# Performance work log

Hardware: AMD Instinct MI355X
Metric: run time of the kernel (lower is better)

Reference implementation:

```python
import jax, jax.numpy as jnp
import numpy as np

B, S, E, H, F = 8, 1024, 1024, 16, 4096
D = E // H  # head_dim = 64
EPS = 1e-5


def setup_inputs() -> dict:
    key = jax.random.key(0)
    ks = jax.random.split(key, 12)
    s = 0.02
    return {
        "x": jax.random.normal(ks[0], (B, S, E), dtype=jnp.float32),
        # per-head projections (shared across heads), torch stores [out,in]; we use [in,out]
        "Wq": jax.random.normal(ks[1], (D, D), dtype=jnp.float32) * s,
        "Wk": jax.random.normal(ks[2], (D, D), dtype=jnp.float32) * s,
        "Wv": jax.random.normal(ks[3], (D, D), dtype=jnp.float32) * s,
        "Wo": jax.random.normal(ks[4], (E, E), dtype=jnp.float32) * s,
        "bo": jnp.zeros((E,), dtype=jnp.float32),
        "W1": jax.random.normal(ks[5], (E, F), dtype=jnp.float32) * s,
        "b1": jnp.zeros((F,), dtype=jnp.float32),
        "W2": jax.random.normal(ks[6], (F, E), dtype=jnp.float32) * s,
        "b2": jnp.zeros((E,), dtype=jnp.float32),
        "g1": jnp.ones((E,), dtype=jnp.float32),
        "beta1": jnp.zeros((E,), dtype=jnp.float32),
        "g2": jnp.ones((E,), dtype=jnp.float32),
        "beta2": jnp.zeros((E,), dtype=jnp.float32),
    }


def _layer_norm(x, g, b):
    m = jnp.mean(x, axis=-1, keepdims=True)
    v = jnp.mean(jnp.square(x - m), axis=-1, keepdims=True)
    return (x - m) * jax.lax.rsqrt(v + EPS) * g + b


def reference(x, Wq, Wk, Wv, Wo, bo, W1, b1, W2, b2, g1, beta1, g2, beta2):
    b, s, e = x.shape
    # --- attention sublayer (pre-norm) ---
    nx = _layer_norm(x, g1, beta1)
    h = nx.reshape(b, s, H, D)              # [B,S,H,D]
    q = h @ Wq                               # per-head linear, weight shared over heads
    k = h @ Wk
    v = h @ Wv
    energy = jnp.einsum('bqhd,bkhd->bhqk', q, k)  # full [B,H,S,S] scores
    mask = jnp.tril(jnp.ones((s, s), dtype=bool))
    energy = jnp.where(mask, energy, -jnp.inf)
    att = jax.nn.softmax(energy / jnp.sqrt(jnp.float32(e)), axis=-1)  # NOTE: scale by sqrt(embed_dim)
    o = jnp.einsum('bhqk,bkhd->bqhd', att, v).reshape(b, s, e)
    x = x + (o @ Wo + bo)
    # --- MLP sublayer (pre-norm); dropout is identity in eval ---
    nx = _layer_norm(x, g2, beta2)
    x = x + (jax.nn.relu(nx @ W1 + b1) @ W2 + b2)
    return x
```

## Files before the change

### kernel.cpp

```cpp
#include <hip/hip_runtime.h>

typedef unsigned short u16;
typedef __attribute__((ext_vector_type(4))) float f4;
typedef __attribute__((ext_vector_type(8))) short s8v;
typedef __attribute__((ext_vector_type(4))) unsigned short u16x4;

#define DEVINL __device__ __forceinline__

DEVINL float b2f(u16 u) { union { unsigned i; float f; } x; x.i = ((unsigned)u) << 16; return x.f; }
DEVINL u16 f2b(float f) {
  union { float f; unsigned i; } x; x.f = f;
  unsigned r = 0x7FFFu + ((x.i >> 16) & 1u);
  return (u16)((x.i + r) >> 16);
}

#define GLD_LDS16(g, l)                                                        \
  __builtin_amdgcn_global_load_lds((__attribute__((address_space(1))) void*)(g), \
                                   (__attribute__((address_space(3))) void*)(l), 16, 0, 0)

__global__ __launch_bounds__(256) void k_transpose(const float* __restrict__ in,
                                                   u16* __restrict__ out, int R, int C) {
  __shared__ float t[32][33];
  int tx = threadIdx.x & 31, ty = threadIdx.x >> 5;
  int c0 = blockIdx.x * 32, r0 = blockIdx.y * 32;
#pragma unroll
  for (int i = 0; i < 32; i += 8)
    t[ty + i][tx] = in[(long)(r0 + ty + i) * C + (c0 + tx)];
  __syncthreads();
#pragma unroll
  for (int i = 0; i < 32; i += 8)
    out[(long)(c0 + ty + i) * R + (r0 + tx)] = f2b(t[tx][ty + i]);
}

__global__ __launch_bounds__(256) void k_vtrans(const u16* __restrict__ v, u16* __restrict__ vt) {
  __shared__ u16 t[64][72];
  int bh = blockIdx.x, b = bh >> 4, h = bh & 15;
  int s0 = blockIdx.y * 64;
  int tid = threadIdx.x;
#pragma unroll
  for (int p = 0; p < 2; ++p) {
    int idx = p * 256 + tid;
    int sl = idx >> 3, c8 = (idx & 7) * 8;
    *(s8v*)(&t[sl][c8]) = *(const s8v*)(v + (((long)(b * 1024 + s0 + sl) * 16 + h) * 64) + c8);
  }
  __syncthreads();
#pragma unroll
  for (int p = 0; p < 2; ++p) {
    int idx = p * 256 + tid;
    int d = idx >> 3, c8 = (idx & 7) * 8;
    s8v o;
#pragma unroll
    for (int e = 0; e < 8; ++e) o[e] = (short)t[c8 + e][d];
    *(s8v*)(vt + ((long)bh * 64 + d) * 1024 + s0 + c8) = o;
  }
}

__global__ __launch_bounds__(256) void k_layernorm(const float* __restrict__ x,
                                                   const float* __restrict__ g,
                                                   const float* __restrict__ be,
                                                   u16* __restrict__ out) {
  long row = blockIdx.x;
  int tid = threadIdx.x;
  f4 v = ((const f4*)(x + row * 1024))[tid];
  float s = v[0] + v[1] + v[2] + v[3];
  float s2 = v[0] * v[0] + v[1] * v[1] + v[2] * v[2] + v[3] * v[3];
#pragma unroll
  for (int off = 32; off > 0; off >>= 1) {
    s += __shfl_down(s, off, 64);
    s2 += __shfl_down(s2, off, 64);
  }
  __shared__ float red[8];
  int wv = tid >> 6, ln = tid & 63;
  if (ln == 0) { red[wv] = s; red[4 + wv] = s2; }
  __syncthreads();
  s = red[0] + red[1] + red[2] + red[3];
  s2 = red[4] + red[5] + red[6] + red[7];
  float mean = s * (1.0f / 1024.0f);
  float var = s2 * (1.0f / 1024.0f) - mean * mean;
  float rs = rsqrtf(var + 1e-5f);
  f4 gg = ((const f4*)g)[tid];
  f4 bb = ((const f4*)be)[tid];
  u16x4 o;
#pragma unroll
  for (int i = 0; i < 4; ++i) o[i] = f2b((v[i] - mean) * rs * gg[i] + bb[i]);
  ((u16x4*)(out + row * 1024))[tid] = o;
}

__global__ __launch_bounds__(256) void k_qkv(const u16* __restrict__ nx, const u16* __restrict__ WqT,
                                             const u16* __restrict__ WkT, const u16* __restrict__ WvT,
                                             u16* __restrict__ q, u16* __restrict__ k,
                                             u16* __restrict__ v) {
  int tid = threadIdx.x, lane = tid & 63, wave = tid >> 6;
  int quad = lane >> 4, l16 = lane & 15;
  long rbase = (long)blockIdx.x * 64 + wave * 16;
  s8v a0 = *(const s8v*)(nx + (rbase + l16) * 64 + quad * 8);
  s8v a1 = *(const s8v*)(nx + (rbase + l16) * 64 + 32 + quad * 8);
  const u16* Ws[3] = {WqT, WkT, WvT};
  u16* Os[3] = {q, k, v};
#pragma unroll
  for (int t = 0; t < 3; ++t) {
#pragma unroll
    for (int j = 0; j < 4; ++j) {
      s8v b0 = *(const s8v*)(Ws[t] + (j * 16 + l16) * 64 + quad * 8);
      s8v b1 = *(const s8v*)(Ws[t] + (j * 16 + l16) * 64 + 32 + quad * 8);
      f4 acc = {0.f, 0.f, 0.f, 0.f};
      acc = __builtin_amdgcn_mfma_f32_16x16x32_bf16(a0, b0, acc, 0, 0, 0);
      acc = __builtin_amdgcn_mfma_f32_16x16x32_bf16(a1, b1, acc, 0, 0, 0);
#pragma unroll
      for (int r = 0; r < 4; ++r)
        Os[t][(rbase + quad * 4 + r) * 64 + j * 16 + l16] = f2b(acc[r]);
    }
  }
}

__global__ __launch_bounds__(256) void k_attn_mfma(const u16* __restrict__ q,
                                                   const u16* __restrict__ kk,
                                                   const u16* __restrict__ vt,
                                                   u16* __restrict__ o) {
  constexpr int LDK = 72;
  __shared__ u16 Ks[64 * LDK];
  __shared__ u16 Vt[64 * LDK];
  __shared__ u16 Ps[4][16 * LDK];
  int tid = threadIdx.x, lane = tid & 63, wave = tid >> 6;
  int quad = lane >> 4, l16 = lane & 15;
  int b = blockIdx.x >> 4, h = blockIdx.x & 15;
  int qi = (int)gridDim.y - 1 - (int)blockIdx.y;
  int q0 = qi * 64 + wave * 16;

  const u16* qp = q + (((long)(b * 1024 + q0 + l16)) * 16 + h) * 64;
  s8v aq0 = *(const s8v*)(qp + quad * 8);
  s8v aq1 = *(const s8v*)(qp + 32 + quad * 8);

  f4 O[4];
  float m_[4], l_[4];
#pragma unroll
  for (int jd = 0; jd < 4; ++jd) O[jd] = f4{0.f, 0.f, 0.f, 0.f};
#pragma unroll
  for (int r = 0; r < 4; ++r) { m_[r] = -__builtin_inff(); l_[r] = 0.f; }

  for (int kt = 0; kt <= qi; ++kt) {
    __syncthreads();
#pragma unroll
    for (int p = 0; p < 2; ++p) {
      int idx = p * 256 + tid;
      int row = idx >> 3, c8 = (idx & 7) * 8;
      *(s8v*)(Ks + row * LDK + c8) =
          *(const s8v*)(kk + (((long)(b * 1024 + kt * 64 + row)) * 16 + h) * 64 + c8);
      *(s8v*)(Vt + row * LDK + c8) =
          *(const s8v*)(vt + ((long)blockIdx.x * 64 + row) * 1024 + kt * 64 + c8);
    }
    __syncthreads();

    f4 sf[4];
#pragma unroll
    for (int jn = 0; jn < 4; ++jn) {
      s8v b0 = *(const s8v*)(Ks + (jn * 16 + l16) * LDK + quad * 8);
      s8v b1 = *(const s8v*)(Ks + (jn * 16 + l16) * LDK + 32 + quad * 8);
      f4 acc = f4{0.f, 0.f, 0.f, 0.f};
      acc = __builtin_amdgcn_mfma_f32_16x16x32_bf16(aq0, b0, acc, 0, 0, 0);
      acc = __builtin_amdgcn_mfma_f32_16x16x32_bf16(aq1, b1, acc, 0, 0, 0);
      sf[jn] = acc;
    }
    bool diag = (kt == qi);
    float rm[4];
#pragma unroll
    for (int r = 0; r < 4; ++r) rm[r] = -__builtin_inff();
#pragma unroll
    for (int jn = 0; jn < 4; ++jn)
#pragma unroll
      for (int r = 0; r < 4; ++r) {
        float v = sf[jn][r] * 0.03125f;
        if (diag && (jn * 16 + l16 > wave * 16 + quad * 4 + r)) v = -__builtin_inff();
        sf[jn][r] = v;
        rm[r] = fmaxf(rm[r], v);
      }
#pragma unroll
    for (int off = 1; off < 16; off <<= 1)
#pragma unroll
      for (int r = 0; r < 4; ++r) rm[r] = fmaxf(rm[r], __shfl_xor(rm[r], off, 64));
    float alpha[4], rs[4];
#pragma unroll
    for (int r = 0; r < 4; ++r) {
      float mn = fmaxf(m_[r], rm[r]);
      alpha[r] = __expf(m_[r] - mn);
      m_[r] = mn;
      rs[r] = 0.f;
    }
#pragma unroll
    for (int jn = 0; jn < 4; ++jn)
#pragma unroll
      for (int r = 0; r < 4; ++r) {
        float p = __expf(sf[jn][r] - m_[r]);
        rs[r] += p;
        Ps[wave][(quad * 4 + r) * LDK + jn * 16 + l16] = f2b(p);
      }
#pragma unroll
    for (int off = 1; off < 16; off <<= 1)
#pragma unroll
      for (int r = 0; r < 4; ++r) rs[r] += __shfl_xor(rs[r], off, 64);
#pragma unroll
    for (int r = 0; r < 4; ++r) l_[r] = l_[r] * alpha[r] + rs[r];
#pragma unroll
    for (int jd = 0; jd < 4; ++jd)
#pragma unroll
      for (int r = 0; r < 4; ++r) O[jd][r] *= alpha[r];
    asm volatile("s_waitcnt lgkmcnt(0)" ::: "memory");
    s8v p0 = *(const s8v*)(&Ps[wave][l16 * LDK + quad * 8]);
    s8v p1 = *(const s8v*)(&Ps[wave][l16 * LDK + 32 + quad * 8]);
#pragma unroll
    for (int jd = 0; jd < 4; ++jd) {
      s8v b0 = *(const s8v*)(Vt + (jd * 16 + l16) * LDK + quad * 8);
      s8v b1 = *(const s8v*)(Vt + (jd * 16 + l16) * LDK + 32 + quad * 8);
      O[jd] = __builtin_amdgcn_mfma_f32_16x16x32_bf16(p0, b0, O[jd], 0, 0, 0);
      O[jd] = __builtin_amdgcn_mfma_f32_16x16x32_bf16(p1, b1, O[jd], 0, 0, 0);
    }
  }
#pragma unroll
  for (int r = 0; r < 4; ++r) {
    float inv = 1.0f / l_[r];
    u16* op = o + (((long)(b * 1024 + q0 + quad * 4 + r)) * 16 + h) * 64;
#pragma unroll
    for (int jd = 0; jd < 4; ++jd) op[jd * 16 + l16] = f2b(O[jd][r] * inv);
  }
}

template <int EPI>
__global__ __launch_bounds__(256) void k_gemm_bt(const u16* __restrict__ A, const u16* __restrict__ BT,
                                                 const float* __restrict__ bias,
                                                 const float* __restrict__ resid,
                                                 void* __restrict__ outp, int M, int N, int K) {
  __shared__ u16 sA[3][128 * 32];
  __shared__ u16 sB[3][128 * 32];
  int tid = threadIdx.x, lane = tid & 63, wave = tid >> 6;
  int quad = lane >> 4, l16 = lane & 15;
  int wm = wave >> 1, wn = wave & 1;
  long bm = blockIdx.x, bn = blockIdx.y;
  int srow = tid >> 2, scol = (tid & 3) * 8;
  const u16* ga = A + (bm * 128 + srow) * (long)K + scol;
  const u16* gb = BT + (bn * 128 + srow) * (long)K + scol;
  int woff = wave * 1024;

  f4 acc[4][4];
#pragma unroll
  for (int i = 0; i < 4; ++i)
#pragma unroll
    for (int j = 0; j < 4; ++j) acc[i][j] = f4{0.f, 0.f, 0.f, 0.f};

#pragma unroll
  for (int t = 0; t < 2; ++t) {
    char* lA = (char*)&sA[t][0] + woff;
    char* lB = (char*)&sB[t][0] + woff;
    GLD_LDS16(ga + t * 32, lA);
    GLD_LDS16(ga + 64 * (long)K + t * 32, lA + 4096);
    GLD_LDS16(gb + t * 32, lB);
    GLD_LDS16(gb + 64 * (long)K + t * 32, lB + 4096);
  }

  int cur = 0;
  for (int k0 = 0; k0 < K; k0 += 32) {
    int k2 = k0 + 64;
    if (k2 < K) {
      asm volatile("s_waitcnt vmcnt(4)\n\ts_barrier" ::: "memory");
      int nb = cur >= 1 ? cur - 1 : 2;
      char* lA = (char*)&sA[nb][0] + woff;
      char* lB = (char*)&sB[nb][0] + woff;
      GLD_LDS16(ga + k2, lA);
      GLD_LDS16(ga + 64 * (long)K + k2, lA + 4096);
      GLD_LDS16(gb + k2, lB);
      GLD_LDS16(gb + 64 * (long)K + k2, lB + 4096);
    } else {
      asm volatile("s_waitcnt vmcnt(0)\n\ts_barrier" ::: "memory");
    }
    const u16* cA = sA[cur];
    const u16* cB = sB[cur];
    s8v aF[4], bF[4];
#pragma unroll
    for (int i = 0; i < 4; ++i)
      aF[i] = *(const s8v*)(cA + (wm * 64 + i * 16 + l16) * 32 + quad * 8);
#pragma unroll
    for (int j = 0; j < 4; ++j)
      bF[j] = *(const s8v*)(cB + (wn * 64 + j * 16 + l16) * 32 + quad * 8);
#pragma unroll
    for (int i = 0; i < 4; ++i)
#pragma unroll
      for (int j = 0; j < 4; ++j)
        acc[i][j] = __builtin_amdgcn_mfma_f32_16x16x32_bf16(aF[i], bF[j], acc[i][j], 0, 0, 0);
    cur = cur < 2 ? cur + 1 : 0;
  }

#pragma unroll
  for (int i = 0; i < 4; ++i) {
#pragma unroll
    for (int j = 0; j < 4; ++j) {
      long row = bm * 128 + wm * 64 + i * 16 + quad * 4;
      int col = (int)bn * 128 + wn * 64 + j * 16 + l16;
      float bcol = bias[col];
#pragma unroll
      for (int r = 0; r < 4; ++r) {
        float val = acc[i][j][r] + bcol;
        if (EPI == 1) {
          ((u16*)outp)[(row + r) * (long)N + col] = f2b(val > 0.f ? val : 0.f);
        } else {
          ((float*)outp)[(row + r) * (long)N + col] = resid[(row + r) * (long)N + col] + val;
        }
      }
    }
  }
}

extern "C" void kernel_launch(void* const* d_in, const int* in_sizes, int n_in, void* d_out,
                              int out_size, void* d_ws, size_t ws_size, hipStream_t stream) {
  const float* x = (const float*)d_in[0];
  const float* Wq = (const float*)d_in[1];
  const float* Wk = (const float*)d_in[2];
  const float* Wv = (const float*)d_in[3];
  const float* Wo = (const float*)d_in[4];
  const float* bo = (const float*)d_in[5];
  const float* W1 = (const float*)d_in[6];
  const float* b1 = (const float*)d_in[7];
  const float* W2 = (const float*)d_in[8];
  const float* b2 = (const float*)d_in[9];
  const float* g1 = (const float*)d_in[10];
  const float* be1 = (const float*)d_in[11];
  const float* g2 = (const float*)d_in[12];
  const float* be2 = (const float*)d_in[13];

  char* ws = (char*)d_ws;
  const size_t MB = 1ull << 20;
  u16* nx = (u16*)(ws + 0);
  u16* qb = (u16*)(ws + 16 * MB);
  u16* kb = (u16*)(ws + 32 * MB);
  u16* vb = (u16*)(ws + 48 * MB);
  float* x1 = (float*)(ws + 64 * MB);
  u16* h1 = (u16*)(ws + 96 * MB);
  u16* vtr = (u16*)(ws + 96 * MB);
  u16* WoT = (u16*)(ws + 160 * MB);
  u16* W1T = (u16*)(ws + 162 * MB);
  u16* W2T = (u16*)(ws + 170 * MB);
  u16* WqT = (u16*)(ws + 178 * MB);
  u16* WkT = WqT + 64 * 64;
  u16* WvT = WkT + 64 * 64;
  u16* ob = nx;
  u16* nx2 = qb;

  k_transpose<<<dim3(32, 32), 256, 0, stream>>>(Wo, WoT, 1024, 1024);
  k_transpose<<<dim3(128, 32), 256, 0, stream>>>(W1, W1T, 1024, 4096);
  k_transpose<<<dim3(32, 128), 256, 0, stream>>>(W2, W2T, 4096, 1024);
  k_transpose<<<dim3(2, 2), 256, 0, stream>>>(Wq, WqT, 64, 64);
  k_transpose<<<dim3(2, 2), 256, 0, stream>>>(Wk, WkT, 64, 64);
  k_transpose<<<dim3(2, 2), 256, 0, stream>>>(Wv, WvT, 64, 64);

  k_layernorm<<<8192, 256, 0, stream>>>(x, g1, be1, nx);
  k_qkv<<<2048, 256, 0, stream>>>(nx, WqT, WkT, WvT, qb, kb, vb);
  k_vtrans<<<dim3(128, 16), 256, 0, stream>>>(vb, vtr);
  k_attn_mfma<<<dim3(128, 16), 256, 0, stream>>>(qb, kb, vtr, ob);
  k_gemm_bt<2><<<dim3(64, 8), 256, 0, stream>>>(ob, WoT, bo, x, x1, 8192, 1024, 1024);

  k_layernorm<<<8192, 256, 0, stream>>>(x1, g2, be2, nx2);
  k_gemm_bt<1><<<dim3(64, 32), 256, 0, stream>>>(nx2, W1T, b1, nullptr, h1, 8192, 4096, 1024);
  k_gemm_bt<2><<<dim3(64, 8), 256, 0, stream>>>(h1, W2T, b2, x1, d_out, 8192, 1024, 4096);
}
```

Measured before the change: 459.4 us.

## Add 256x256-tile 8-wave pipelined GEMM for the W1 MLP up-projection

Adds a new GEMM kernel using 256x256 output tiles with 512 threads, a double-buffered 128KB LDS fed by global_load_lds, swizzled LDS reads, and a phased schedule that interleaves loads, barriers and MFMA blocks under raised wave priority. Only the first MLP GEMM (8192x4096x1024 with ReLU) uses it. The larger tile raises arithmetic intensity and reduces global traffic, and the phased schedule overlaps memory with compute. In exchange it uses the full LDS, gives one block per CU, and launches only 512 blocks.

```diff
diff --git a/kernel.cpp b/kernel.cpp
--- a/kernel.cpp
+++ b/kernel.cpp
@@ -302,6 +302,161 @@
           ((u16*)outp)[(row + r) * (long)N + col] = f2b(val > 0.f ? val : 0.f);
         } else {
           ((float*)outp)[(row + r) * (long)N + col] = resid[(row + r) * (long)N + col] + val;
+        }
+      }
+    }
+  }
+}
+
+template <int EPI>
+__global__ __launch_bounds__(512) void k_gemm256(const u16* __restrict__ A,
+                                                 const u16* __restrict__ BT,
+                                                 const float* __restrict__ bias,
+                                                 const float* __restrict__ resid,
+                                                 void* __restrict__ outp, int M, int N, int K) {
+  __shared__ __align__(16) u16 S[65536];
+  int tid = threadIdx.x, lane = tid & 63, wave = tid >> 6;
+  int l16 = lane & 15, quad = lane >> 4;
+  int wm = wave >> 2, wn = wave & 3;
+  long bm = blockIdx.x, bn = blockIdx.y;
+
+  int swx = ((l16 >> 3) & 1) << 4;
+  int baseA = (((wm * 64 + l16) * 32) + quad * 8) ^ swx;
+  int baseB = (((wn * 32 + l16) * 32) + quad * 8) ^ swx;
+
+  int Lb = tid * 16;
+  int Ls = Lb ^ (((Lb >> 9) & 1) << 5);
+  int r_ = Ls >> 6, kin = (Ls & 63) >> 1;
+  const u16* pA = A + (bm * 256 + r_) * (long)K + kin;
+  const u16* pB = BT + (bn * 256 + r_) * (long)K + kin;
+
+  f4 acc[4][4][2];
+#pragma unroll
+  for (int q = 0; q < 4; ++q)
+#pragma unroll
+    for (int mi = 0; mi < 4; ++mi)
+#pragma unroll
+      for (int nj = 0; nj < 2; ++nj) acc[q][mi][nj] = f4{0.f, 0.f, 0.f, 0.f};
+  s8v aF[4][2], bF[2][2][2];
+
+#define BAR asm volatile("s_barrier" ::: "memory")
+#define LGK0 asm volatile("s_waitcnt lgkmcnt(0)" ::: "memory")
+#define WVM4 asm volatile("s_waitcnt vmcnt(4)" ::: "memory")
+#define WVM0 asm volatile("s_waitcnt vmcnt(0)" ::: "memory")
+
+#define STAGE(mat, half, t, buf)                                               \
+  do {                                                                         \
+    const u16* g_ = ((mat) ? pB : pA) + (long)(half) * 128 * K + (t) * 64;     \
+    char* l_ = ((char*)S) + ((buf) * 32768 + (mat) * 16384 + (half) * 8192) * 2 + wave * 1024; \
+    GLD_LDS16(g_, l_);                                                         \
+    GLD_LDS16(g_ + 32, l_ + 8192);                                             \
+  } while (0)
+
+#define LDA(buf, mh)                                                           \
+  do {                                                                         \
+    const u16* p_ = S + (buf) * 32768 + (mh) * 8192 + baseA;                   \
+    _Pragma("unroll") for (int mi = 0; mi < 4; ++mi) {                         \
+      aF[mi][0] = *(const s8v*)(p_ + mi * 512);                                \
+      aF[mi][1] = *(const s8v*)(p_ + mi * 512 + 4096);                         \
+    }                                                                          \
+  } while (0)
+
+#define LDB(buf, nh, set)                                                      \
+  do {                                                                         \
+    const u16* p_ = S + (buf) * 32768 + 16384 + (nh) * 8192 + baseB;           \
+    _Pragma("unroll") for (int nj = 0; nj < 2; ++nj) {                         \
+      bF[set][nj][0] = *(const s8v*)(p_ + nj * 512);                           \
+      bF[set][nj][1] = *(const s8v*)(p_ + nj * 512 + 4096);                    \
+    }                                                                          \
+  } while (0)
+
+#define MM(q)                                                                  \
+  do {                                                                         \
+    _Pragma("unroll") for (int mi = 0; mi < 4; ++mi)                           \
+        _Pragma("unroll") for (int nj = 0; nj < 2; ++nj) {                     \
+      acc[q][mi][nj] = __builtin_amdgcn_mfma_f32_16x16x32_bf16(                \
+          aF[mi][0], bF[(q) & 1][nj][0], acc[q][mi][nj], 0, 0, 0);             \
+      acc[q][mi][nj] = __builtin_amdgcn_mfma_f32_16x16x32_bf16(                \
+          aF[mi][1], bF[(q) & 1][nj][1], acc[q][mi][nj], 0, 0, 0);             \
+    }                                                                          \
+  } while (0)
+
+#define PHASES(t, LAST)                                                        \
+                                             \
+  LDA(0, 0); LDB(0, 0, 0); STAGE(0, 1, (t) + 1, 1);                            \
+  BAR; LGK0; __builtin_amdgcn_s_setprio(1); MM(0); __builtin_amdgcn_s_setprio(0); BAR; \
+                                                           \
+  LDB(0, 1, 1); STAGE(1, 1, (t) + 1, 1);                                       \
+  BAR; LGK0; __builtin_amdgcn_s_setprio(1); MM(1); __builtin_amdgcn_s_setprio(0); BAR; \
+                                                           \
+  LDA(0, 1); if (!(LAST)) STAGE(0, 0, (t) + 2, 0);                             \
+  BAR; LGK0; __builtin_amdgcn_s_setprio(1); MM(2); __builtin_amdgcn_s_setprio(0); BAR; \
+                                          \
+  if (!(LAST)) STAGE(1, 0, (t) + 2, 0);                                        \
+  __builtin_amdgcn_s_setprio(1); MM(3); __builtin_amdgcn_s_setprio(0);         \
+  if (LAST) { WVM0; } else { WVM4; }                                           \
+  BAR;                                                                         \
+                                           \
+  LDA(1, 0); LDB(1, 0, 0); if (!(LAST)) STAGE(0, 1, (t) + 2, 0);               \
+  BAR; LGK0; __builtin_amdgcn_s_setprio(1); MM(0); __builtin_amdgcn_s_setprio(0); BAR; \
+                                                           \
+  LDB(1, 1, 1); if (!(LAST)) STAGE(1, 1, (t) + 2, 0);                          \
+  BAR; LGK0; __builtin_amdgcn_s_setprio(1); MM(1); __builtin_amdgcn_s_setprio(0); BAR; \
+                                                           \
+  LDA(1, 1); if (!(LAST)) STAGE(0, 0, (t) + 3, 1);                             \
+  BAR; LGK0; __builtin_amdgcn_s_setprio(1); MM(2); __builtin_amdgcn_s_setprio(0); BAR; \
+                                                           \
+  if (!(LAST)) STAGE(1, 0, (t) + 3, 1);                                        \
+  __builtin_amdgcn_s_setprio(1); MM(3); __builtin_amdgcn_s_setprio(0);         \
+  if (!(LAST)) { WVM4; BAR; }
+
+  STAGE(0, 0, 0, 0);
+  STAGE(1, 0, 0, 0);
+  STAGE(0, 1, 0, 0);
+  STAGE(1, 1, 0, 0);
+  STAGE(0, 0, 1, 1);
+  STAGE(1, 0, 1, 1);
+  WVM4; BAR;
+
+  int NI = K >> 7;
+  for (int i = 0; i < NI - 1; ++i) {
+    int t = 2 * i;
+    PHASES(t, 0);
+  }
+  {
+    int t = 2 * (NI - 1);
+    PHASES(t, 1);
+  }
+
+#undef PHASES
+#undef MM
+#undef LDB
+#undef LDA
+#undef STAGE
+#undef WVM0
+#undef WVM4
+#undef LGK0
+#undef BAR
+
+#pragma unroll
+  for (int q = 0; q < 4; ++q) {
+    int mh = q >> 1, nh = q & 1;
+#pragma unroll
+    for (int mi = 0; mi < 4; ++mi) {
+#pragma unroll
+      for (int nj = 0; nj < 2; ++nj) {
+        long row = bm * 256 + mh * 128 + wm * 64 + mi * 16 + quad * 4;
+        int col = (int)bn * 256 + nh * 128 + wn * 32 + nj * 16 + l16;
+        float bcol = bias[col];
+#pragma unroll
+        for (int rr = 0; rr < 4; ++rr) {
+          float val = acc[q][mi][nj][rr] + bcol;
+          if (EPI == 1) {
+            ((u16*)outp)[(row + rr) * (long)N + col] = f2b(val > 0.f ? val : 0.f);
+          } else {
+            ((float*)outp)[(row + rr) * (long)N + col] =
+                resid[(row + rr) * (long)N + col] + val;
+          }
         }
       }
     }
@@ -357,6 +512,6 @@
   k_gemm_bt<2><<<dim3(64, 8), 256, 0, stream>>>(ob, WoT, bo, x, x1, 8192, 1024, 1024);
 
   k_layernorm<<<8192, 256, 0, stream>>>(x1, g2, be2, nx2);
-  k_gemm_bt<1><<<dim3(64, 32), 256, 0, stream>>>(nx2, W1T, b1, nullptr, h1, 8192, 4096, 1024);
+  k_gemm256<1><<<dim3(32, 16), 512, 0, stream>>>(nx2, W1T, b1, nullptr, h1, 8192, 4096, 1024);
   k_gemm_bt<2><<<dim3(64, 8), 256, 0, stream>>>(h1, W2T, b2, x1, d_out, 8192, 1024, 4096);
 }
```

Result: faster. 448.0 us (-2.5%).
